# Kernel tuning notes

Measured on AMD Instinct MI355X. Metric: run time of the kernel, lower is better.

## Reference

```python
import jax, jax.numpy as jnp
import numpy as np

M, N, C, D = 2, 8, 1024, 256  # n_routers, num_adapters, channel_dim, down_sample_size
B, S = 32, 512


def setup_inputs() -> dict:
    key = jax.random.key(0)
    k1, k2, k3, k4, k5 = jax.random.split(key, 5)
    x = jax.random.normal(k1, (B, S, C), dtype=jnp.float32)
    expert_index = jax.random.randint(k2, (M, B), 0, N, dtype=jnp.int32)
    down_w = jax.random.normal(k3, (M, N, C, D), dtype=jnp.float32) * 0.01
    down_b = jax.random.normal(k4, (M, N, D), dtype=jnp.float32) * 0.01
    up_w = jax.random.normal(k5, (M, N, D, C), dtype=jnp.float32) * 0.01
    return {"x": x, "expert_index": expert_index, "down_w": down_w,
            "down_b": down_b, "up_w": up_w}


def reference(x, expert_index, down_w, down_b, up_w):
    # Gather per-(router, batch-element) adapter weights along the adapter axis.
    idx = expert_index  # [M, B]
    bw_down = jnp.take_along_axis(down_w, idx[:, :, None, None], axis=1)  # [M, B, C, D]
    bb_down = jnp.take_along_axis(down_b, idx[:, :, None], axis=1)        # [M, B, D]
    bw_up = jnp.take_along_axis(up_w, idx[:, :, None, None], axis=1)      # [M, B, D, C]
    # z = swish(x @ W_down + b_down)  -> [M, B, S, D]
    z = jnp.einsum('bsc,mbcd->mbsd', x, bw_down) + bb_down[:, :, None, :]
    z = jax.nn.silu(z)
    # u = z @ W_up -> [M, B, S, C]
    u = jnp.einsum('mbsd,mbdc->mbsc', z, bw_up)
    return u
```

## Files before the change

### kernel.cpp

```cpp
#include <hip/hip_runtime.h>
#include <stdint.h>

typedef unsigned short u16;
typedef __bf16 bf16x8 __attribute__((ext_vector_type(8)));
typedef float f32x4 __attribute__((ext_vector_type(4)));

#define MM 2
#define NN 8
#define CC 1024
#define DD 256
#define BB 32
#define SS 512

__device__ __forceinline__ u16 f2bf(float f) {
  uint32_t u = __float_as_uint(f);
  u += 0x7FFFu + ((u >> 16) & 1u);
  return (u16)(u >> 16);
}

__device__ __forceinline__ uint32_t pack2(float a, float b) {
  return (uint32_t)f2bf(a) | ((uint32_t)f2bf(b) << 16);
}

__device__ __forceinline__ void async16(const void* g, void* l) {
  __builtin_amdgcn_global_load_lds(
      (const __attribute__((address_space(1))) uint32_t*)g,
      (__attribute__((address_space(3))) uint32_t*)l, 16, 0, 0);
}

__global__ __launch_bounds__(256) void prep_w(
    const float* __restrict__ dw, u16* __restrict__ wdT,
    const float* __restrict__ uw, u16* __restrict__ wuT) {
  __shared__ float tile[64][33];
  int bid = blockIdx.x;
  const float* src; u16* dst; int K, N, tk, tn;
  if (bid < 2048) {
    K = CC; N = DD;
    const int slab = bid >> 7, t = bid & 127;
    tk = t >> 3; tn = t & 7;
    src = dw + (size_t)slab * K * N;
    dst = wdT + (size_t)slab * K * N;
  } else {
    bid -= 2048;
    K = DD; N = CC;
    const int slab = bid >> 7, t = bid & 127;
    tk = t >> 5; tn = t & 31;
    src = uw + (size_t)slab * K * N;
    dst = wuT + (size_t)slab * K * N;
  }
  const int k0 = tk * 64, n0 = tn * 32;
  const int tx = threadIdx.x & 31, ty = threadIdx.x >> 5;
#pragma unroll
  for (int i = 0; i < 64; i += 8)
    tile[ty + i][tx] = src[(size_t)(k0 + ty + i) * N + n0 + tx];
  __syncthreads();
  uint32_t* dst32 = reinterpret_cast<uint32_t*>(dst);
#pragma unroll
  for (int i = 0; i < 32; i += 8) {
    const int nr = ty + i;
    dst32[((size_t)(n0 + nr) * K + k0) / 2 + tx] =
        pack2(tile[2 * tx][nr], tile[2 * tx + 1][nr]);
  }
}

__global__ __launch_bounds__(512, 4) void fused_adapter(
    const float* __restrict__ x, const u16* __restrict__ wdT,
    const u16* __restrict__ wuT, const float* __restrict__ db,
    const int* __restrict__ eidx, float* __restrict__ out) {
  __shared__ __align__(16) u16 smA[2][64 * 32];
  __shared__ __align__(16) u16 smB[2][256 * 32];
  __shared__ __align__(16) u16 zl[8 * 64 * 32];

  const int pair = blockIdx.y;
  const int m = pair & 1;
  const int b = pair >> 1;
  const int mb = m * BB + b;
  const int e = eidx[mb];
  const int s0 = blockIdx.x * 64;

  const int tid = threadIdx.x;
  const int lane = tid & 63;
  const int wave = tid >> 6;
  const int quad = lane >> 4;
  const int l16 = lane & 15;
  const int fx = (l16 >> 1) & 3;

  const int wr = (wave >> 2) * 32;
  const int wc = (wave & 3) * 64;

  const u16* Bd = wdT + (size_t)(m * NN + e) * DD * CC;
  const u16* Bu = wuT + (size_t)(m * NN + e) * CC * DD;

  const int arow = tid >> 3;
  const int akseg = (tid & 7) * 4;
  const float* gAx = x + ((size_t)b * SS + s0 + arow) * CC + akseg;
  const int lAoff = arow * 32 +
                    ((((tid & 7) >> 1) ^ ((arow >> 1) & 3)) * 8) + (tid & 1) * 4;

  const int srow = lane >> 2;
  const int qx = (lane & 3) ^ ((srow >> 1) & 3);
  const u16* gB0 = Bd + (size_t)(wave * 32 + srow) * CC + qx * 8;
  const u16* gB1 = gB0 + (size_t)16 * CC;
  const int lB0o = wave * 32 * 32;
  const int lB1o = lB0o + 16 * 32;

  f32x4 acc[2][4];
#pragma unroll
  for (int i = 0; i < 2; ++i)
#pragma unroll
    for (int j = 0; j < 4; ++j) acc[i][j] = (f32x4){0.f, 0.f, 0.f, 0.f};

  {
    float4 a0 = *reinterpret_cast<const float4*>(gAx);
    uint2 w; w.x = pack2(a0.x, a0.y); w.y = pack2(a0.z, a0.w);
    *reinterpret_cast<uint2*>(&smA[0][lAoff]) = w;
  }
  async16(gB0, &smB[0][lB0o]);
  async16(gB1, &smB[0][lB1o]);
  __syncthreads();

  for (int kk = 0; kk < 32; ++kk) {
    const int cur = kk & 1, nxt = cur ^ 1;
    float4 nA;
    if (kk < 31) {
      const int ko = (kk + 1) * 32;
      nA = *reinterpret_cast<const float4*>(gAx + ko);
      async16(gB0 + ko, &smB[nxt][lB0o]);
      async16(gB1 + ko, &smB[nxt][lB1o]);
    } else {
      async16(Bu + (size_t)(wave * 32 + srow) * DD + qx * 8, &smB[nxt][lB0o]);
      async16(Bu + (size_t)(wave * 32 + 16 + srow) * DD + qx * 8, &smB[nxt][lB1o]);
    }
    bf16x8 af[2], bfr[4];
#pragma unroll
    for (int i = 0; i < 2; ++i)
      af[i] = *reinterpret_cast<const bf16x8*>(
          &smA[cur][(wr + i * 16 + l16) * 32 + (quad ^ fx) * 8]);
#pragma unroll
    for (int j = 0; j < 4; ++j)
      bfr[j] = *reinterpret_cast<const bf16x8*>(
          &smB[cur][(wc + j * 16 + l16) * 32 + (quad ^ fx) * 8]);
#pragma unroll
    for (int i = 0; i < 2; ++i)
#pragma unroll
      for (int j = 0; j < 4; ++j)
        acc[i][j] = __builtin_amdgcn_mfma_f32_16x16x32_bf16(af[i], bfr[j], acc[i][j], 0, 0, 0);
    if (kk < 31) {
      uint2 w; w.x = pack2(nA.x, nA.y); w.y = pack2(nA.z, nA.w);
      *reinterpret_cast<uint2*>(&smA[nxt][lAoff]) = w;
    }
    __syncthreads();
  }

  const float* bias_p = db + (size_t)(m * NN + e) * DD;
#pragma unroll
  for (int j = 0; j < 4; ++j) {
    const int d = wc + j * 16 + l16;
    const float bias = bias_p[d];
    const int kt = d >> 5;
    const int kl = d & 31;
    const int slot0 = kl >> 3;
    const int kin = kl & 7;
#pragma unroll
    for (int i = 0; i < 2; ++i) {
      const int zr = wr + i * 16 + quad * 4;
#pragma unroll
      for (int r = 0; r < 4; ++r) {
        const int row = zr + r;
        float v = acc[i][j][r] + bias;
        v = v / (1.f + __expf(-v));
        zl[kt * 2048 + row * 32 + ((slot0 ^ ((row >> 1) & 3)) * 8) + kin] = f2bf(v);
      }
    }
  }
  __syncthreads();

  float* ob = out + ((size_t)mb * SS + s0) * CC;

  for (int g = 0; g < 32; ++g) {
    const int cur2 = g & 1, nxt2 = cur2 ^ 1;
    const int ct = g >> 3;
    const int it = g & 7;
    if (g < 31) {
      const int g2 = g + 1;
      const int ct2 = g2 >> 3;
      const int io2 = (g2 & 7) * 32;
      async16(Bu + (size_t)(ct2 * 256 + wave * 32 + srow) * DD + io2 + qx * 8,
              &smB[nxt2][lB0o]);
      async16(Bu + (size_t)(ct2 * 256 + wave * 32 + 16 + srow) * DD + io2 + qx * 8,
              &smB[nxt2][lB1o]);
    }
    if (it == 0) {
#pragma unroll
      for (int i = 0; i < 2; ++i)
#pragma unroll
        for (int j = 0; j < 4; ++j) acc[i][j] = (f32x4){0.f, 0.f, 0.f, 0.f};
    }
    bf16x8 af[2], bfr[4];
#pragma unroll
    for (int i = 0; i < 2; ++i)
      af[i] = *reinterpret_cast<const bf16x8*>(
          &zl[it * 2048 + (wr + i * 16 + l16) * 32 + (quad ^ fx) * 8]);
#pragma unroll
    for (int j = 0; j < 4; ++j)
      bfr[j] = *reinterpret_cast<const bf16x8*>(
          &smB[cur2][(wc + j * 16 + l16) * 32 + (quad ^ fx) * 8]);
#pragma unroll
    for (int i = 0; i < 2; ++i)
#pragma unroll
      for (int j = 0; j < 4; ++j)
        acc[i][j] = __builtin_amdgcn_mfma_f32_16x16x32_bf16(af[i], bfr[j], acc[i][j], 0, 0, 0);
    if (it == 7) {
#pragma unroll
      for (int j = 0; j < 4; ++j) {
        const int c = ct * 256 + wc + j * 16 + l16;
#pragma unroll
        for (int i = 0; i < 2; ++i) {
          const int sr = wr + i * 16 + quad * 4;
#pragma unroll
          for (int r = 0; r < 4; ++r)
            ob[(size_t)(sr + r) * CC + c] = acc[i][j][r];
        }
      }
    }
    __syncthreads();
  }
}

extern "C" void kernel_launch(void* const* d_in, const int* in_sizes, int n_in,
                              void* d_out, int out_size, void* d_ws, size_t ws_size,
                              hipStream_t stream) {
  const float* x  = (const float*)d_in[0];
  const int* eidx = (const int*)d_in[1];
  const float* dw = (const float*)d_in[2];
  const float* db = (const float*)d_in[3];
  const float* uw = (const float*)d_in[4];
  float* out = (float*)d_out;

  char* ws = (char*)d_ws;
  u16* wdT = (u16*)(ws);
  u16* wuT = (u16*)(ws + (size_t)8 * 1024 * 1024);

  prep_w<<<dim3(4096), dim3(256), 0, stream>>>(dw, wdT, uw, wuT);
  fused_adapter<<<dim3(SS / 64, MM * BB), dim3(512), 0, stream>>>(
      x, wdT, wuT, db, eidx, out);
}
```

Before: 278.7 us.

## Double row tile to 128 with triple-buffered weight pipeline and counted waits

Doubles the sequence tile per block from 64 to 128 rows, so each wave computes a 64x64 output tile and each weight tile loaded into LDS is reused across twice as many rows. Weight tiles move to a three-slot ring prefetched two steps ahead, and __syncthreads is replaced with explicit vmcnt waits plus s_barrier so loads stay in flight across barriers. The bias load is also hoisted to the start of the kernel. The costs are roughly double the LDS and accumulator registers per block, a lower occupancy target (launch bound 2), and half as many blocks. The hand-counted vmcnt values depend on exactly how many loads are outstanding, which is fragile.

```diff
diff --git a/kernel.cpp b/kernel.cpp
--- a/kernel.cpp
+++ b/kernel.cpp
@@ -63,20 +63,19 @@
   }
 }
 
-__global__ __launch_bounds__(512, 4) void fused_adapter(
+__global__ __launch_bounds__(512, 2) void fused_adapter(
     const float* __restrict__ x, const u16* __restrict__ wdT,
     const u16* __restrict__ wuT, const float* __restrict__ db,
     const int* __restrict__ eidx, float* __restrict__ out) {
-  __shared__ __align__(16) u16 smA[2][64 * 32];
-  __shared__ __align__(16) u16 smB[2][256 * 32];
-  __shared__ __align__(16) u16 zl[8 * 64 * 32];
+  __shared__ __align__(16) u16 smA[2][128 * 32];
+  __shared__ __align__(16) u16 smB[3][256 * 32];
+  __shared__ __align__(16) u16 zl[8 * 128 * 32];
 
   const int pair = blockIdx.y;
-  const int m = pair & 1;
-  const int b = pair >> 1;
-  const int mb = m * BB + b;
-  const int e = eidx[mb];
-  const int s0 = blockIdx.x * 64;
+  const int m = pair >> 5;
+  const int b = pair & 31;
+  const int e = eidx[pair];
+  const int s0 = blockIdx.x * 128;
 
   const int tid = threadIdx.x;
   const int lane = tid & 63;
@@ -85,128 +84,141 @@
   const int l16 = lane & 15;
   const int fx = (l16 >> 1) & 3;
 
-  const int wr = (wave >> 2) * 32;
+  const int wr = (wave >> 2) * 64;
   const int wc = (wave & 3) * 64;
 
   const u16* Bd = wdT + (size_t)(m * NN + e) * DD * CC;
   const u16* Bu = wuT + (size_t)(m * NN + e) * CC * DD;
 
-  const int arow = tid >> 3;
-  const int akseg = (tid & 7) * 4;
-  const float* gAx = x + ((size_t)b * SS + s0 + arow) * CC + akseg;
-  const int lAoff = arow * 32 +
-                    ((((tid & 7) >> 1) ^ ((arow >> 1) & 3)) * 8) + (tid & 1) * 4;
+  const float* bias_p = db + (size_t)(m * NN + e) * DD;
+  float biasr[4];
+#pragma unroll
+  for (int j = 0; j < 4; ++j) biasr[j] = bias_p[wc + j * 16 + l16];
+
+  const int arow = tid >> 2;
+  const int achk = tid & 3;
+  const float* gAx = x + ((size_t)b * SS + s0 + arow) * CC + achk * 8;
+  const int lAoff = arow * 32 + ((achk ^ ((arow >> 1) & 3)) * 8);
 
   const int srow = lane >> 2;
   const int qx = (lane & 3) ^ ((srow >> 1) & 3);
-  const u16* gB0 = Bd + (size_t)(wave * 32 + srow) * CC + qx * 8;
-  const u16* gB1 = gB0 + (size_t)16 * CC;
+  const u16* gBd = Bd + (size_t)(wave * 32 + srow) * CC + qx * 8;
+  const u16* gBu = Bu + (size_t)(wave * 32 + srow) * DD + qx * 8;
   const int lB0o = wave * 32 * 32;
   const int lB1o = lB0o + 16 * 32;
 
-  f32x4 acc[2][4];
-#pragma unroll
-  for (int i = 0; i < 2; ++i)
+  f32x4 acc[4][4];
+#pragma unroll
+  for (int i = 0; i < 4; ++i)
 #pragma unroll
     for (int j = 0; j < 4; ++j) acc[i][j] = (f32x4){0.f, 0.f, 0.f, 0.f};
 
   {
     float4 a0 = *reinterpret_cast<const float4*>(gAx);
-    uint2 w; w.x = pack2(a0.x, a0.y); w.y = pack2(a0.z, a0.w);
-    *reinterpret_cast<uint2*>(&smA[0][lAoff]) = w;
-  }
-  async16(gB0, &smB[0][lB0o]);
-  async16(gB1, &smB[0][lB1o]);
-  __syncthreads();
+    float4 a1 = *reinterpret_cast<const float4*>(gAx + 4);
+    async16(gBd, &smB[0][lB0o]);
+    async16(gBd + 16 * CC, &smB[0][lB1o]);
+    async16(gBd + 32, &smB[1][lB0o]);
+    async16(gBd + 16 * CC + 32, &smB[1][lB1o]);
+    *reinterpret_cast<uint4*>(&smA[0][lAoff]) =
+        make_uint4(pack2(a0.x, a0.y), pack2(a0.z, a0.w),
+                   pack2(a1.x, a1.y), pack2(a1.z, a1.w));
+  }
+  asm volatile("s_waitcnt vmcnt(2) lgkmcnt(0)" ::: "memory");
+  __builtin_amdgcn_s_barrier();
 
   for (int kk = 0; kk < 32; ++kk) {
-    const int cur = kk & 1, nxt = cur ^ 1;
-    float4 nA;
+    const int slot = kk % 3, nslot = (kk + 2) % 3;
+    const int abuf = kk & 1;
+    float4 nA0, nA1;
     if (kk < 31) {
       const int ko = (kk + 1) * 32;
-      nA = *reinterpret_cast<const float4*>(gAx + ko);
-      async16(gB0 + ko, &smB[nxt][lB0o]);
-      async16(gB1 + ko, &smB[nxt][lB1o]);
+      nA0 = *reinterpret_cast<const float4*>(gAx + ko);
+      nA1 = *reinterpret_cast<const float4*>(gAx + ko + 4);
+    }
+    if (kk < 30) {
+      const int ko2 = (kk + 2) * 32;
+      async16(gBd + ko2, &smB[nslot][lB0o]);
+      async16(gBd + 16 * CC + ko2, &smB[nslot][lB1o]);
     } else {
-      async16(Bu + (size_t)(wave * 32 + srow) * DD + qx * 8, &smB[nxt][lB0o]);
-      async16(Bu + (size_t)(wave * 32 + 16 + srow) * DD + qx * 8, &smB[nxt][lB1o]);
-    }
-    bf16x8 af[2], bfr[4];
-#pragma unroll
-    for (int i = 0; i < 2; ++i)
+      const int g = kk - 30;
+      async16(gBu + g * 32, &smB[nslot][lB0o]);
+      async16(gBu + 16 * DD + g * 32, &smB[nslot][lB1o]);
+    }
+    bf16x8 af[4], bfr[4];
+#pragma unroll
+    for (int i = 0; i < 4; ++i)
       af[i] = *reinterpret_cast<const bf16x8*>(
-          &smA[cur][(wr + i * 16 + l16) * 32 + (quad ^ fx) * 8]);
+          &smA[abuf][(wr + i * 16 + l16) * 32 + (quad ^ fx) * 8]);
 #pragma unroll
     for (int j = 0; j < 4; ++j)
       bfr[j] = *reinterpret_cast<const bf16x8*>(
-          &smB[cur][(wc + j * 16 + l16) * 32 + (quad ^ fx) * 8]);
-#pragma unroll
-    for (int i = 0; i < 2; ++i)
+          &smB[slot][(wc + j * 16 + l16) * 32 + (quad ^ fx) * 8]);
+#pragma unroll
+    for (int i = 0; i < 4; ++i)
 #pragma unroll
       for (int j = 0; j < 4; ++j)
         acc[i][j] = __builtin_amdgcn_mfma_f32_16x16x32_bf16(af[i], bfr[j], acc[i][j], 0, 0, 0);
     if (kk < 31) {
-      uint2 w; w.x = pack2(nA.x, nA.y); w.y = pack2(nA.z, nA.w);
-      *reinterpret_cast<uint2*>(&smA[nxt][lAoff]) = w;
-    }
-    __syncthreads();
-  }
-
-  const float* bias_p = db + (size_t)(m * NN + e) * DD;
+      *reinterpret_cast<uint4*>(&smA[abuf ^ 1][lAoff]) =
+          make_uint4(pack2(nA0.x, nA0.y), pack2(nA0.z, nA0.w),
+                     pack2(nA1.x, nA1.y), pack2(nA1.z, nA1.w));
+    }
+    asm volatile("s_waitcnt vmcnt(2) lgkmcnt(0)" ::: "memory");
+    __builtin_amdgcn_s_barrier();
+  }
+
 #pragma unroll
   for (int j = 0; j < 4; ++j) {
     const int d = wc + j * 16 + l16;
-    const float bias = bias_p[d];
     const int kt = d >> 5;
     const int kl = d & 31;
     const int slot0 = kl >> 3;
     const int kin = kl & 7;
 #pragma unroll
-    for (int i = 0; i < 2; ++i) {
+    for (int i = 0; i < 4; ++i) {
       const int zr = wr + i * 16 + quad * 4;
 #pragma unroll
       for (int r = 0; r < 4; ++r) {
         const int row = zr + r;
-        float v = acc[i][j][r] + bias;
+        float v = acc[i][j][r] + biasr[j];
         v = v / (1.f + __expf(-v));
-        zl[kt * 2048 + row * 32 + ((slot0 ^ ((row >> 1) & 3)) * 8) + kin] = f2bf(v);
+        zl[kt * 4096 + row * 32 + ((slot0 ^ ((row >> 1) & 3)) * 8) + kin] = f2bf(v);
       }
     }
   }
-  __syncthreads();
-
-  float* ob = out + ((size_t)mb * SS + s0) * CC;
+  asm volatile("s_waitcnt vmcnt(2) lgkmcnt(0)" ::: "memory");
+  __builtin_amdgcn_s_barrier();
+
+  float* ob = out + ((size_t)pair * SS + s0) * CC;
 
   for (int g = 0; g < 32; ++g) {
-    const int cur2 = g & 1, nxt2 = cur2 ^ 1;
+    const int slot = (g + 2) % 3, nslot = (g + 1) % 3;
     const int ct = g >> 3;
     const int it = g & 7;
-    if (g < 31) {
-      const int g2 = g + 1;
-      const int ct2 = g2 >> 3;
-      const int io2 = (g2 & 7) * 32;
-      async16(Bu + (size_t)(ct2 * 256 + wave * 32 + srow) * DD + io2 + qx * 8,
-              &smB[nxt2][lB0o]);
-      async16(Bu + (size_t)(ct2 * 256 + wave * 32 + 16 + srow) * DD + io2 + qx * 8,
-              &smB[nxt2][lB1o]);
+    if (g < 30) {
+      const int g2 = g + 2;
+      const size_t ro = (size_t)(g2 >> 3) * 256 * DD + (g2 & 7) * 32;
+      async16(gBu + ro, &smB[nslot][lB0o]);
+      async16(gBu + ro + 16 * DD, &smB[nslot][lB1o]);
     }
     if (it == 0) {
 #pragma unroll
-      for (int i = 0; i < 2; ++i)
+      for (int i = 0; i < 4; ++i)
 #pragma unroll
         for (int j = 0; j < 4; ++j) acc[i][j] = (f32x4){0.f, 0.f, 0.f, 0.f};
     }
-    bf16x8 af[2], bfr[4];
-#pragma unroll
-    for (int i = 0; i < 2; ++i)
+    bf16x8 af[4], bfr[4];
+#pragma unroll
+    for (int i = 0; i < 4; ++i)
       af[i] = *reinterpret_cast<const bf16x8*>(
-          &zl[it * 2048 + (wr + i * 16 + l16) * 32 + (quad ^ fx) * 8]);
+          &zl[it * 4096 + (wr + i * 16 + l16) * 32 + (quad ^ fx) * 8]);
 #pragma unroll
     for (int j = 0; j < 4; ++j)
       bfr[j] = *reinterpret_cast<const bf16x8*>(
-          &smB[cur2][(wc + j * 16 + l16) * 32 + (quad ^ fx) * 8]);
-#pragma unroll
-    for (int i = 0; i < 2; ++i)
+          &smB[slot][(wc + j * 16 + l16) * 32 + (quad ^ fx) * 8]);
+#pragma unroll
+    for (int i = 0; i < 4; ++i)
 #pragma unroll
       for (int j = 0; j < 4; ++j)
         acc[i][j] = __builtin_amdgcn_mfma_f32_16x16x32_bf16(af[i], bfr[j], acc[i][j], 0, 0, 0);
@@ -215,7 +227,7 @@
       for (int j = 0; j < 4; ++j) {
         const int c = ct * 256 + wc + j * 16 + l16;
 #pragma unroll
-        for (int i = 0; i < 2; ++i) {
+        for (int i = 0; i < 4; ++i) {
           const int sr = wr + i * 16 + quad * 4;
 #pragma unroll
           for (int r = 0; r < 4; ++r)
@@ -223,7 +235,15 @@
         }
       }
     }
-    __syncthreads();
+    if (g < 31) {
+      if (g == 30)
+        asm volatile("s_waitcnt vmcnt(0) lgkmcnt(0)" ::: "memory");
+      else if (it == 7)
+        asm volatile("s_waitcnt vmcnt(18) lgkmcnt(0)" ::: "memory");
+      else
+        asm volatile("s_waitcnt vmcnt(2) lgkmcnt(0)" ::: "memory");
+      __builtin_amdgcn_s_barrier();
+    }
   }
 }
 
@@ -242,6 +262,6 @@
   u16* wuT = (u16*)(ws + (size_t)8 * 1024 * 1024);
 
   prep_w<<<dim3(4096), dim3(256), 0, stream>>>(dw, wdT, uw, wuT);
-  fused_adapter<<<dim3(SS / 64, MM * BB), dim3(512), 0, stream>>>(
+  fused_adapter<<<dim3(SS / 128, MM * BB), dim3(512), 0, stream>>>(
       x, wdT, wuT, db, eidx, out);
 }
```

Result: faster. 268.8 us (-3.6%).
